# Kernel optimization log

Measured on AMD Instinct MI355X. Metric: run time of the kernel, lower is better.

## Reference

```python
import jax, jax.numpy as jnp
import numpy as np

N = 4096
DIN = 512
H = 128    # hidden_dim per head
K = 4      # num_heads
DOUT = 16  # output classes
ALPHA = 0.2  # leaky relu negative slope


def setup_inputs() -> dict:
    key = jax.random.key(0)
    ks = jax.random.split(key, 8)
    X = jax.random.normal(ks[0], (N, DIN), jnp.float32)
    # sparse random graph (p=0.01), non-zero where edges exist
    adj = (jax.random.uniform(ks[1], (N, N)) < 0.01).astype(jnp.float32)
    W1 = jax.random.normal(ks[2], (K, DIN, H), jnp.float32) * np.float32(1.0 / np.sqrt(DIN))
    a_src1 = jax.random.normal(ks[3], (K, H), jnp.float32) * np.float32(0.1)
    a_dst1 = jax.random.normal(ks[4], (K, H), jnp.float32) * np.float32(0.1)
    W2 = jax.random.normal(ks[5], (K * H, DOUT), jnp.float32) * np.float32(1.0 / np.sqrt(K * H))
    a_src2 = jax.random.normal(ks[6], (DOUT,), jnp.float32) * np.float32(0.1)
    a_dst2 = jax.random.normal(ks[7], (DOUT,), jnp.float32) * np.float32(0.1)
    return {"X": X, "adj": adj, "W1": W1, "a_src1": a_src1, "a_dst1": a_dst1,
            "W2": W2, "a_src2": a_src2, "a_dst2": a_dst2}


def gat_multihead(h, mask, W, a_src, a_dst):
    # h: (N, Din), W: (K, Din, O), a_src/a_dst: (K, O), mask: (N, N) bool
    Wh = jnp.einsum('ni,kio->kno', h, W)                      # (K, N, O)
    src = jnp.einsum('kno,ko->kn', Wh, a_src)                 # (K, N)
    dst = jnp.einsum('kno,ko->kn', Wh, a_dst)                 # (K, N)
    e = jax.nn.leaky_relu(src[:, :, None] + dst[:, None, :], ALPHA)  # (K, N, N)
    e = jnp.where(mask[None], e, -jnp.inf)
    attn = jax.nn.softmax(e, axis=-1)                         # rows sum to 1 (self-loop guarantees >=1 edge)
    return jnp.einsum('knm,kmo->kno', attn, Wh)               # (K, N, O)


def reference(X, adj, W1, a_src1, a_dst1, W2, a_src2, a_dst2):
    # mask = (adj + I) > 0
    mask = (adj + jnp.eye(N, dtype=adj.dtype)) > 0
    # layer 1: 4 heads, concatenated, then ELU (eval mode: no dropout)
    h1 = gat_multihead(X, mask, W1, a_src1, a_dst1)           # (K, N, H)
    h1 = jnp.transpose(h1, (1, 0, 2)).reshape(N, K * H)       # concat heads -> (N, K*H)
    h1 = jax.nn.elu(h1)
    # layer 2: single head, mean over heads == the head itself
    h2 = gat_multihead(h1, mask, W2[None], a_src2[None], a_dst2[None])[0]  # (N, DOUT)
    return jax.nn.log_softmax(h2, axis=1)
```

## Files before the change

### kernel.cpp

```cpp
#include <hip/hip_runtime.h>
#include <hip/hip_bf16.h>
#include <hip/hip_fp16.h>


typedef __attribute__((ext_vector_type(4))) float floatx4;
typedef __attribute__((ext_vector_type(8))) short short8;
typedef __attribute__((ext_vector_type(4))) unsigned short ushortx4;
typedef __attribute__((ext_vector_type(4))) unsigned int uintx4;
typedef unsigned short u16b;

#define GN 4096
#define LDP 40

__device__ __forceinline__ u16b f2bf(float f) {
  union { float f; unsigned int i; } v; v.f = f;
  unsigned int r = v.i + 0x7FFF + ((v.i >> 16) & 1);
  return (u16b)(r >> 16);
}
__device__ __forceinline__ float bflo(unsigned u) {
  union { unsigned i; float f; } v; v.i = u << 16; return v.f;
}
__device__ __forceinline__ float bfhi(unsigned u) {
  union { unsigned i; float f; } v; v.i = u & 0xffff0000u; return v.f;
}
__device__ __forceinline__ float h2f(unsigned short h) {
  return __half2float(__ushort_as_half(h));
}

__global__ __launch_bounds__(512) void k_mask(const float* __restrict__ adj,
                                              u16b* __restrict__ mask) {
  int t = threadIdx.x;
  int n = blockIdx.x * 2 + (t >> 8);
  int cg = t & 255;
  const float* ap = adj + (size_t)n * 4096 + cg * 16;
  floatx4 v0 = *(const floatx4*)(ap);
  floatx4 v1 = *(const floatx4*)(ap + 4);
  floatx4 v2 = *(const floatx4*)(ap + 8);
  floatx4 v3 = *(const floatx4*)(ap + 12);
  unsigned bits = 0;
#pragma unroll
  for (int i = 0; i < 4; ++i) {
    bits |= (unsigned)(v0[i] != 0.f) << i;
    bits |= (unsigned)(v1[i] != 0.f) << (4 + i);
    bits |= (unsigned)(v2[i] != 0.f) << (8 + i);
    bits |= (unsigned)(v3[i] != 0.f) << (12 + i);
  }
  if ((n >> 4) == cg) bits |= 1u << (n & 15);
  mask[(size_t)n * 256 + cg] = (u16b)bits;
}

__global__ __launch_bounds__(512) void k_gemm1(const float* __restrict__ X,
    const float* __restrict__ W1, const float* __restrict__ as1,
    const float* __restrict__ ad1, u16b* __restrict__ Wh1bf,
    float* __restrict__ src1t, float* __restrict__ dst1t) {
  int b = blockIdx.x, t = threadIdx.x;
  int lane = t & 63, w = t >> 6;
  __shared__ u16b Ab[64 * LDP];
  __shared__ u16b Bb[128 * LDP];
  __shared__ float sps[4][64], sds[4][64];
  int p = ((b >> 5) << 3) | (b & 7);
  int hd = (b >> 3) & 3;
  int rb = p * 64;
  const float* Wk = W1 + (size_t)hd * 65536;
  int wr = w >> 2, wc = w & 3, lh = lane >> 4, lm = lane & 15;
  int ar = t >> 2, aq = t & 3;
  int u = t - 256, kk0 = (u & 7) * 4, c0 = (u >> 3) * 4;
  floatx4 pa0, pa1, pb0, pb1, pb2, pb3;
  if (t < 256) {
    const float* ap = X + (size_t)(rb + ar) * 512 + aq * 8;
    pa0 = *(const floatx4*)(ap);
    pa1 = *(const floatx4*)(ap + 4);
  } else {
    const float* bp = Wk + (size_t)kk0 * 128 + c0;
    pb0 = *(const floatx4*)(bp);
    pb1 = *(const floatx4*)(bp + 128);
    pb2 = *(const floatx4*)(bp + 256);
    pb3 = *(const floatx4*)(bp + 384);
  }
  floatx4 acc[2][2] = {};
  for (int kk = 0; kk < 512; kk += 32) {
    if (t < 256) {
      short8 a;
      a[0] = (short)f2bf(pa0[0]); a[1] = (short)f2bf(pa0[1]);
      a[2] = (short)f2bf(pa0[2]); a[3] = (short)f2bf(pa0[3]);
      a[4] = (short)f2bf(pa1[0]); a[5] = (short)f2bf(pa1[1]);
      a[6] = (short)f2bf(pa1[2]); a[7] = (short)f2bf(pa1[3]);
      *(short8*)(&Ab[ar * LDP + aq * 8]) = a;
    } else {
#pragma unroll
      for (int cq = 0; cq < 4; ++cq) {
        ushortx4 v;
        v[0] = f2bf(pb0[cq]); v[1] = f2bf(pb1[cq]);
        v[2] = f2bf(pb2[cq]); v[3] = f2bf(pb3[cq]);
        *(ushortx4*)(&Bb[(c0 + cq) * LDP + kk0]) = v;
      }
    }
    __syncthreads();
    if (kk + 32 < 512) {
      if (t < 256) {
        const float* ap = X + (size_t)(rb + ar) * 512 + kk + 32 + aq * 8;
        pa0 = *(const floatx4*)(ap);
        pa1 = *(const floatx4*)(ap + 4);
      } else {
        const float* bp = Wk + (size_t)(kk + 32 + kk0) * 128 + c0;
        pb0 = *(const floatx4*)(bp);
        pb1 = *(const floatx4*)(bp + 128);
        pb2 = *(const floatx4*)(bp + 256);
        pb3 = *(const floatx4*)(bp + 384);
      }
    }
    short8 a0 = *(const short8*)(&Ab[(wr * 32      + lm) * LDP + lh * 8]);
    short8 a1 = *(const short8*)(&Ab[(wr * 32 + 16 + lm) * LDP + lh * 8]);
    short8 b0 = *(const short8*)(&Bb[(wc * 32      + lm) * LDP + lh * 8]);
    short8 b1 = *(const short8*)(&Bb[(wc * 32 + 16 + lm) * LDP + lh * 8]);
    acc[0][0] = __builtin_amdgcn_mfma_f32_16x16x32_bf16(a0, b0, acc[0][0], 0, 0, 0);
    acc[0][1] = __builtin_amdgcn_mfma_f32_16x16x32_bf16(a0, b1, acc[0][1], 0, 0, 0);
    acc[1][0] = __builtin_amdgcn_mfma_f32_16x16x32_bf16(a1, b0, acc[1][0], 0, 0, 0);
    acc[1][1] = __builtin_amdgcn_mfma_f32_16x16x32_bf16(a1, b1, acc[1][1], 0, 0, 0);
    __syncthreads();
  }
#pragma unroll
  for (int m = 0; m < 2; ++m)
#pragma unroll
    for (int n2 = 0; n2 < 2; ++n2)
#pragma unroll
      for (int j = 0; j < 4; ++j)
        Wh1bf[(size_t)(rb + wr * 32 + m * 16 + lh * 4 + j) * 512
              + hd * 128 + wc * 32 + n2 * 16 + lm] = f2bf(acc[m][n2][j]);
  float asv[2], adv[2];
#pragma unroll
  for (int n2 = 0; n2 < 2; ++n2) {
    asv[n2] = as1[hd * 128 + wc * 32 + n2 * 16 + lm];
    adv[n2] = ad1[hd * 128 + wc * 32 + n2 * 16 + lm];
  }
#pragma unroll
  for (int m = 0; m < 2; ++m)
#pragma unroll
    for (int j = 0; j < 4; ++j) {
      float ps = acc[m][0][j] * asv[0] + acc[m][1][j] * asv[1];
      float pd = acc[m][0][j] * adv[0] + acc[m][1][j] * adv[1];
#pragma unroll
      for (int off = 8; off >= 1; off >>= 1) {
        ps += __shfl_xor(ps, off, 16);
        pd += __shfl_xor(pd, off, 16);
      }
      if (lm == 0) {
        sps[wc][wr * 32 + m * 16 + lh * 4 + j] = ps;
        sds[wc][wr * 32 + m * 16 + lh * 4 + j] = pd;
      }
    }
  __syncthreads();
  if (t < 64) {
    src1t[(size_t)(rb + t) * 4 + hd] = sps[0][t] + sps[1][t] + sps[2][t] + sps[3][t];
    dst1t[(size_t)(rb + t) * 4 + hd] = sds[0][t] + sds[1][t] + sds[2][t] + sds[3][t];
  }
}

__global__ __launch_bounds__(256) void k_attn1(const u16b* __restrict__ mask,
    const u16b* __restrict__ Wh1bf,
    const float* __restrict__ src1t, const float* __restrict__ dst1t,
    const float* __restrict__ W2, const float* __restrict__ as2,
    const float* __restrict__ ad2, float* __restrict__ Wh2,
    float* __restrict__ src2, float* __restrict__ dst2) {
  int w = threadIdx.x >> 6, lane = threadIdx.x & 63;
  int n = blockIdx.x * 4 + w;
  __shared__ u16b lst4[4][512];
  __shared__ unsigned short ewh4[4][2048];
  __shared__ float h1t4[4][512];
  u16b* lst = lst4[w];
  unsigned short* ewh = ewh4[w];
  float* h1t = h1t4[w];
  unsigned long long B = *(const unsigned long long*)((const char*)mask + (size_t)n * 512 + lane * 8);
  int pc = __popcll(B);
  int incl = pc;
#pragma unroll
  for (int off = 1; off <= 32; off <<= 1) {
    int v = __shfl_up(incl, off);
    if (lane >= off) incl += v;
  }
  int cnt = __shfl(incl, 63);
  int pos = incl - pc;
  while (B) {
    int c = __builtin_ctzll(B);
    lst[pos++] = (u16b)(lane * 64 + c);
    B &= B - 1;
  }
  floatx4 sn = *(const floatx4*)(src1t + (size_t)n * 4);
  float mx[4], sm[4];
#pragma unroll
  for (int k = 0; k < 4; ++k) { mx[k] = -1e30f; sm[k] = 0.f; }
  for (int li = lane; li < cnt; li += 64) {
    int m = lst[li];
    floatx4 dv = *(const floatx4*)(dst1t + (size_t)m * 4);
    ushortx4 ev;
#pragma unroll
    for (int k = 0; k < 4; ++k) {
      float e = sn[k] + dv[k];
      e = e > 0.f ? e : 0.2f * e;
      ev[k] = __half_as_ushort(__float2half(e));
      if (e > mx[k]) { sm[k] = sm[k] * __expf(mx[k] - e) + 1.f; mx[k] = e; }
      else sm[k] += __expf(e - mx[k]);
    }
    *(ushortx4*)(&ewh[li * 4]) = ev;
  }
#pragma unroll
  for (int k = 0; k < 4; ++k) {
#pragma unroll
    for (int off = 32; off >= 1; off >>= 1) {
      float mo = __shfl_xor(mx[k], off);
      float so = __shfl_xor(sm[k], off);
      float M = fmaxf(mx[k], mo);
      sm[k] = sm[k] * __expf(mx[k] - M) + so * __expf(mo - M);
      mx[k] = M;
    }
    sm[k] = 1.f / sm[k];
  }
  for (int li = lane; li < cnt; li += 64) {
    ushortx4 ev = *(const ushortx4*)(&ewh[li * 4]);
#pragma unroll
    for (int k = 0; k < 4; ++k) {
      float e = h2f(ev[k]);
      ev[k] = __half_as_ushort(__float2half(__expf(e - mx[k]) * sm[k]));
    }
    *(ushortx4*)(&ewh[li * 4]) = ev;
  }
  int hd = lane >> 4;
  const char* gb = (const char*)Wh1bf + lane * 16;
  float a[8] = {0.f, 0.f, 0.f, 0.f, 0.f, 0.f, 0.f, 0.f};
  int mreg[8];
  float wreg[8];
  int nfull = cnt >> 3;
  if (nfull) {
#pragma unroll
    for (int q = 0; q < 8; ++q) {
      mreg[q] = lst[q];
      wreg[q] = h2f(ewh[q * 4 + hd]);
    }
  }
  for (int c = 0; c < nfull; ++c) {
    uintx4 u0 = *(const uintx4*)(gb + (size_t)mreg[0] * 1024);
    uintx4 u1 = *(const uintx4*)(gb + (size_t)mreg[1] * 1024);
    uintx4 u2 = *(const uintx4*)(gb + (size_t)mreg[2] * 1024);
    uintx4 u3 = *(const uintx4*)(gb + (size_t)mreg[3] * 1024);
    uintx4 u4 = *(const uintx4*)(gb + (size_t)mreg[4] * 1024);
    uintx4 u5 = *(const uintx4*)(gb + (size_t)mreg[5] * 1024);
    uintx4 u6 = *(const uintx4*)(gb + (size_t)mreg[6] * 1024);
    uintx4 u7 = *(const uintx4*)(gb + (size_t)mreg[7] * 1024);
    float f0 = wreg[0], f1 = wreg[1], f2 = wreg[2], f3 = wreg[3];
    float f4 = wreg[4], f5 = wreg[5], f6 = wreg[6], f7 = wreg[7];
    if (c + 1 < nfull) {
      int nb = (c + 1) * 8;
#pragma unroll
      for (int q = 0; q < 8; ++q) {
        mreg[q] = lst[nb + q];
        wreg[q] = h2f(ewh[(nb + q) * 4 + hd]);
      }
    }
#pragma unroll
    for (int j = 0; j < 4; ++j) {
      a[2*j]   = fmaf(f0, bflo(u0[j]), a[2*j]); a[2*j+1] = fmaf(f0, bfhi(u0[j]), a[2*j+1]);
    }
#pragma unroll
    for (int j = 0; j < 4; ++j) {
      a[2*j]   = fmaf(f1, bflo(u1[j]), a[2*j]); a[2*j+1] = fmaf(f1, bfhi(u1[j]), a[2*j+1]);
    }
#pragma unroll
    for (int j = 0; j < 4; ++j) {
      a[2*j]   = fmaf(f2, bflo(u2[j]), a[2*j]); a[2*j+1] = fmaf(f2, bfhi(u2[j]), a[2*j+1]);
    }
#pragma unroll
    for (int j = 0; j < 4; ++j) {
      a[2*j]   = fmaf(f3, bflo(u3[j]), a[2*j]); a[2*j+1] = fmaf(f3, bfhi(u3[j]), a[2*j+1]);
    }
#pragma unroll
    for (int j = 0; j < 4; ++j) {
      a[2*j]   = fmaf(f4, bflo(u4[j]), a[2*j]); a[2*j+1] = fmaf(f4, bfhi(u4[j]), a[2*j+1]);
    }
#pragma unroll
    for (int j = 0; j < 4; ++j) {
      a[2*j]   = fmaf(f5, bflo(u5[j]), a[2*j]); a[2*j+1] = fmaf(f5, bfhi(u5[j]), a[2*j+1]);
    }
#pragma unroll
    for (int j = 0; j < 4; ++j) {
      a[2*j]   = fmaf(f6, bflo(u6[j]), a[2*j]); a[2*j+1] = fmaf(f6, bfhi(u6[j]), a[2*j+1]);
    }
#pragma unroll
    for (int j = 0; j < 4; ++j) {
      a[2*j]   = fmaf(f7, bflo(u7[j]), a[2*j]); a[2*j+1] = fmaf(f7, bfhi(u7[j]), a[2*j+1]);
    }
  }
  for (int li = nfull * 8; li < cnt; ++li) {
    int m = lst[li];
    float wv = h2f(ewh[li * 4 + hd]);
    uintx4 u = *(const uintx4*)(gb + (size_t)m * 1024);
#pragma unroll
    for (int j = 0; j < 4; ++j) {
      a[2*j]   = fmaf(wv, bflo(u[j]), a[2*j]);
      a[2*j+1] = fmaf(wv, bfhi(u[j]), a[2*j+1]);
    }
  }
#pragma unroll
  for (int j = 0; j < 8; ++j) {
    float v = a[j];
    h1t[j * 64 + lane] = v > 0.f ? v : __expf(v) - 1.f;
  }
  int o = lane & 15, ig = lane >> 4;
  float p0 = 0.f, p1 = 0.f, p2 = 0.f, p3 = 0.f;
  for (int j = 0; j < 128; j += 4) {
    int i0 = ig + 4 * j;
    int i1 = i0 + 4, i2 = i0 + 8, i3 = i0 + 12;
    p0 = fmaf(h1t[(i0 & 7) * 64 + (i0 >> 3)], W2[i0 * 16 + o], p0);
    p1 = fmaf(h1t[(i1 & 7) * 64 + (i1 >> 3)], W2[i1 * 16 + o], p1);
    p2 = fmaf(h1t[(i2 & 7) * 64 + (i2 >> 3)], W2[i2 * 16 + o], p2);
    p3 = fmaf(h1t[(i3 & 7) * 64 + (i3 >> 3)], W2[i3 * 16 + o], p3);
  }
  float pacc = (p0 + p1) + (p2 + p3);
  pacc += __shfl_xor(pacc, 16);
  pacc += __shfl_xor(pacc, 32);
  if (lane < 16) {
    Wh2[(size_t)n * 16 + lane] = pacc;
    float ps = pacc * as2[lane];
    float pd = pacc * ad2[lane];
#pragma unroll
    for (int off = 8; off >= 1; off >>= 1) {
      ps += __shfl_xor(ps, off, 16);
      pd += __shfl_xor(pd, off, 16);
    }
    if (lane == 0) { src2[n] = ps; dst2[n] = pd; }
  }
}

__global__ __launch_bounds__(256) void k_attn2(const u16b* __restrict__ mask,
    const float* __restrict__ Wh2, const float* __restrict__ src2,
    const float* __restrict__ dst2, float* __restrict__ out) {
  int w = threadIdx.x >> 6, lane = threadIdx.x & 63;
  int n = blockIdx.x * 4 + w;
  __shared__ int2 pr4[4][512];
  int2* pr = pr4[w];
  float snv = src2[n];
  unsigned long long B = *(const unsigned long long*)((const char*)mask + (size_t)n * 512 + lane * 8);
  int pc = __popcll(B);
  int incl = pc;
#pragma unroll
  for (int off = 1; off <= 32; off <<= 1) {
    int v = __shfl_up(incl, off);
    if (lane >= off) incl += v;
  }
  int cnt = __shfl(incl, 63);
  int pos = incl - pc;
  float mx = -1e30f, sm = 0.f;
  while (B) {
    int c = __builtin_ctzll(B);
    int m = lane * 64 + c;
    float e = snv + dst2[m];
    e = e > 0.f ? e : 0.2f * e;
    if (e > mx) { sm = sm * __expf(mx - e) + 1.f; mx = e; }
    else sm += __expf(e - mx);
    int2 pv; pv.x = m << 4; pv.y = __float_as_int(e);
    pr[pos++] = pv;
    B &= B - 1;
  }
#pragma unroll
  for (int off = 32; off >= 1; off >>= 1) {
    float mo = __shfl_xor(mx, off);
    float so = __shfl_xor(sm, off);
    float M = fmaxf(mx, mo);
    sm = sm * __expf(mx - M) + so * __expf(mo - M);
    mx = M;
  }
  float R = 1.f / sm;
  int o = lane & 15, g = lane >> 4;
  float acc = 0.f;
  for (int li = g; li < cnt; li += 4) {
    int2 pv = pr[li];
    float wgt = __expf(__int_as_float(pv.y) - mx) * R;
    acc = fmaf(wgt, Wh2[pv.x + o], acc);
  }
  acc += __shfl_xor(acc, 16);
  acc += __shfl_xor(acc, 32);
  float vm = acc;
#pragma unroll
  for (int off = 8; off >= 1; off >>= 1) vm = fmaxf(vm, __shfl_xor(vm, off, 16));
  float ex = __expf(acc - vm);
#pragma unroll
  for (int off = 8; off >= 1; off >>= 1) ex += __shfl_xor(ex, off, 16);
  if (lane < 16) out[(size_t)n * 16 + lane] = acc - vm - __logf(ex);
}

extern "C" void kernel_launch(void* const* d_in, const int* in_sizes, int n_in,
                              void* d_out, int out_size, void* d_ws, size_t ws_size,
                              hipStream_t stream) {
  const float* X   = (const float*)d_in[0];
  const float* adj = (const float*)d_in[1];
  const float* W1  = (const float*)d_in[2];
  const float* as1 = (const float*)d_in[3];
  const float* ad1 = (const float*)d_in[4];
  const float* W2  = (const float*)d_in[5];
  const float* as2 = (const float*)d_in[6];
  const float* ad2 = (const float*)d_in[7];
  float* out = (float*)d_out;

  char* ws = (char*)d_ws;
  float* src1t = (float*)ws;
  float* dst1t = (float*)(ws + (64 << 10));
  float* src2  = (float*)(ws + (128 << 10));
  float* dst2  = (float*)(ws + (144 << 10));
  float* Wh2   = (float*)(ws + (160 << 10));
  u16b*  mask  = (u16b*)(ws + (512 << 10));
  u16b*  Wh1bf = (u16b*)(ws + (4ull << 20));

  k_mask <<<dim3(2048), dim3(512), 0, stream>>>(adj, mask);
  k_gemm1<<<dim3(256),  dim3(512), 0, stream>>>(X, W1, as1, ad1, Wh1bf, src1t, dst1t);
  k_attn1<<<dim3(1024), dim3(256), 0, stream>>>(mask, Wh1bf, src1t, dst1t,
                                                W2, as2, ad2, Wh2, src2, dst2);
  k_attn2<<<dim3(1024), dim3(256), 0, stream>>>(mask, Wh2, src2, dst2, out);
}
```

Baseline: 61.63 us.

## Merge mask and GEMM kernels into one launch; double-buffer attn1 gathers

Folds the adjacency-to-bitmask kernel and the layer-1 GEMM into a single launch, with block ranges split by role, so the two independent stages overlap and one launch is saved. In the layer-1 aggregation, the neighbor list is zero-padded to an even number of 8-element chunks, removing the scalar tail loop. The gather loop now keeps two register sets of eight rows, loading the next chunk while the current one is accumulated. This hides gather latency but raises register pressure and does some padded work on row 0 with zero weight.

```diff
diff --git a/kernel.cpp b/kernel.cpp
--- a/kernel.cpp
+++ b/kernel.cpp
@@ -27,132 +27,131 @@
   return __half2float(__ushort_as_half(h));
 }
 
-__global__ __launch_bounds__(512) void k_mask(const float* __restrict__ adj,
-                                              u16b* __restrict__ mask) {
-  int t = threadIdx.x;
-  int n = blockIdx.x * 2 + (t >> 8);
-  int cg = t & 255;
-  const float* ap = adj + (size_t)n * 4096 + cg * 16;
-  floatx4 v0 = *(const floatx4*)(ap);
-  floatx4 v1 = *(const floatx4*)(ap + 4);
-  floatx4 v2 = *(const floatx4*)(ap + 8);
-  floatx4 v3 = *(const floatx4*)(ap + 12);
-  unsigned bits = 0;
-#pragma unroll
-  for (int i = 0; i < 4; ++i) {
-    bits |= (unsigned)(v0[i] != 0.f) << i;
-    bits |= (unsigned)(v1[i] != 0.f) << (4 + i);
-    bits |= (unsigned)(v2[i] != 0.f) << (8 + i);
-    bits |= (unsigned)(v3[i] != 0.f) << (12 + i);
-  }
-  if ((n >> 4) == cg) bits |= 1u << (n & 15);
-  mask[(size_t)n * 256 + cg] = (u16b)bits;
-}
-
-__global__ __launch_bounds__(512) void k_gemm1(const float* __restrict__ X,
-    const float* __restrict__ W1, const float* __restrict__ as1,
-    const float* __restrict__ ad1, u16b* __restrict__ Wh1bf,
+__global__ __launch_bounds__(512) void k_fused1(const float* __restrict__ adj,
+    const float* __restrict__ X, const float* __restrict__ W1,
+    const float* __restrict__ as1, const float* __restrict__ ad1,
+    u16b* __restrict__ mask, u16b* __restrict__ Wh1bf,
     float* __restrict__ src1t, float* __restrict__ dst1t) {
   int b = blockIdx.x, t = threadIdx.x;
   int lane = t & 63, w = t >> 6;
-  __shared__ u16b Ab[64 * LDP];
-  __shared__ u16b Bb[128 * LDP];
-  __shared__ float sps[4][64], sds[4][64];
-  int p = ((b >> 5) << 3) | (b & 7);
-  int hd = (b >> 3) & 3;
-  int rb = p * 64;
-  const float* Wk = W1 + (size_t)hd * 65536;
-  int wr = w >> 2, wc = w & 3, lh = lane >> 4, lm = lane & 15;
-  int ar = t >> 2, aq = t & 3;
-  int u = t - 256, kk0 = (u & 7) * 4, c0 = (u >> 3) * 4;
-  floatx4 pa0, pa1, pb0, pb1, pb2, pb3;
-  if (t < 256) {
-    const float* ap = X + (size_t)(rb + ar) * 512 + aq * 8;
-    pa0 = *(const floatx4*)(ap);
-    pa1 = *(const floatx4*)(ap + 4);
+  if (b >= 256) {
+    int n = (b - 256) * 2 + (t >> 8);
+    int cg = t & 255;
+    const float* ap = adj + (size_t)n * 4096 + cg * 16;
+    floatx4 v0 = *(const floatx4*)(ap);
+    floatx4 v1 = *(const floatx4*)(ap + 4);
+    floatx4 v2 = *(const floatx4*)(ap + 8);
+    floatx4 v3 = *(const floatx4*)(ap + 12);
+    unsigned bits = 0;
+#pragma unroll
+    for (int i = 0; i < 4; ++i) {
+      bits |= (unsigned)(v0[i] != 0.f) << i;
+      bits |= (unsigned)(v1[i] != 0.f) << (4 + i);
+      bits |= (unsigned)(v2[i] != 0.f) << (8 + i);
+      bits |= (unsigned)(v3[i] != 0.f) << (12 + i);
+    }
+    if ((n >> 4) == cg) bits |= 1u << (n & 15);
+    mask[(size_t)n * 256 + cg] = (u16b)bits;
   } else {
-    const float* bp = Wk + (size_t)kk0 * 128 + c0;
-    pb0 = *(const floatx4*)(bp);
-    pb1 = *(const floatx4*)(bp + 128);
-    pb2 = *(const floatx4*)(bp + 256);
-    pb3 = *(const floatx4*)(bp + 384);
-  }
-  floatx4 acc[2][2] = {};
-  for (int kk = 0; kk < 512; kk += 32) {
+    __shared__ u16b Ab[64 * LDP];
+    __shared__ u16b Bb[128 * LDP];
+    __shared__ float sps[4][64], sds[4][64];
+    int p = ((b >> 5) << 3) | (b & 7);
+    int hd = (b >> 3) & 3;
+    int rb = p * 64;
+    const float* Wk = W1 + (size_t)hd * 65536;
+    int wr = w >> 2, wc = w & 3, lh = lane >> 4, lm = lane & 15;
+    int ar = t >> 2, aq = t & 3;
+    int u = t - 256, kk0 = (u & 7) * 4, c0 = (u >> 3) * 4;
+    floatx4 pa0, pa1, pb0, pb1, pb2, pb3;
     if (t < 256) {
-      short8 a;
-      a[0] = (short)f2bf(pa0[0]); a[1] = (short)f2bf(pa0[1]);
-      a[2] = (short)f2bf(pa0[2]); a[3] = (short)f2bf(pa0[3]);
-      a[4] = (short)f2bf(pa1[0]); a[5] = (short)f2bf(pa1[1]);
-      a[6] = (short)f2bf(pa1[2]); a[7] = (short)f2bf(pa1[3]);
-      *(short8*)(&Ab[ar * LDP + aq * 8]) = a;
+      const float* ap = X + (size_t)(rb + ar) * 512 + aq * 8;
+      pa0 = *(const floatx4*)(ap);
+      pa1 = *(const floatx4*)(ap + 4);
     } else {
-#pragma unroll
-      for (int cq = 0; cq < 4; ++cq) {
-        ushortx4 v;
-        v[0] = f2bf(pb0[cq]); v[1] = f2bf(pb1[cq]);
-        v[2] = f2bf(pb2[cq]); v[3] = f2bf(pb3[cq]);
-        *(ushortx4*)(&Bb[(c0 + cq) * LDP + kk0]) = v;
-      }
-    }
+      const float* bp = Wk + (size_t)kk0 * 128 + c0;
+      pb0 = *(const floatx4*)(bp);
+      pb1 = *(const floatx4*)(bp + 128);
+      pb2 = *(const floatx4*)(bp + 256);
+      pb3 = *(const floatx4*)(bp + 384);
+    }
+    floatx4 acc[2][2] = {};
+    for (int kk = 0; kk < 512; kk += 32) {
+      if (t < 256) {
+        short8 a;
+        a[0] = (short)f2bf(pa0[0]); a[1] = (short)f2bf(pa0[1]);
+        a[2] = (short)f2bf(pa0[2]); a[3] = (short)f2bf(pa0[3]);
+        a[4] = (short)f2bf(pa1[0]); a[5] = (short)f2bf(pa1[1]);
+        a[6] = (short)f2bf(pa1[2]); a[7] = (short)f2bf(pa1[3]);
+        *(short8*)(&Ab[ar * LDP + aq * 8]) = a;
+      } else {
+#pragma unroll
+        for (int cq = 0; cq < 4; ++cq) {
+          ushortx4 v;
+          v[0] = f2bf(pb0[cq]); v[1] = f2bf(pb1[cq]);
+          v[2] = f2bf(pb2[cq]); v[3] = f2bf(pb3[cq]);
+          *(ushortx4*)(&Bb[(c0 + cq) * LDP + kk0]) = v;
+        }
+      }
+      __syncthreads();
+      if (kk + 32 < 512) {
+        if (t < 256) {
+          const float* ap = X + (size_t)(rb + ar) * 512 + kk + 32 + aq * 8;
+          pa0 = *(const floatx4*)(ap);
+          pa1 = *(const floatx4*)(ap + 4);
+        } else {
+          const float* bp = Wk + (size_t)(kk + 32 + kk0) * 128 + c0;
+          pb0 = *(const floatx4*)(bp);
+          pb1 = *(const floatx4*)(bp + 128);
+          pb2 = *(const floatx4*)(bp + 256);
+          pb3 = *(const floatx4*)(bp + 384);
+        }
+      }
+      short8 a0 = *(const short8*)(&Ab[(wr * 32      + lm) * LDP + lh * 8]);
+      short8 a1 = *(const short8*)(&Ab[(wr * 32 + 16 + lm) * LDP + lh * 8]);
+      short8 b0 = *(const short8*)(&Bb[(wc * 32      + lm) * LDP + lh * 8]);
+      short8 b1 = *(const short8*)(&Bb[(wc * 32 + 16 + lm) * LDP + lh * 8]);
+      acc[0][0] = __builtin_amdgcn_mfma_f32_16x16x32_bf16(a0, b0, acc[0][0], 0, 0, 0);
+      acc[0][1] = __builtin_amdgcn_mfma_f32_16x16x32_bf16(a0, b1, acc[0][1], 0, 0, 0);
+      acc[1][0] = __builtin_amdgcn_mfma_f32_16x16x32_bf16(a1, b0, acc[1][0], 0, 0, 0);
+      acc[1][1] = __builtin_amdgcn_mfma_f32_16x16x32_bf16(a1, b1, acc[1][1], 0, 0, 0);
+      __syncthreads();
+    }
+#pragma unroll
+    for (int m = 0; m < 2; ++m)
+#pragma unroll
+      for (int n2 = 0; n2 < 2; ++n2)
+#pragma unroll
+        for (int j = 0; j < 4; ++j)
+          Wh1bf[(size_t)(rb + wr * 32 + m * 16 + lh * 4 + j) * 512
+                + hd * 128 + wc * 32 + n2 * 16 + lm] = f2bf(acc[m][n2][j]);
+    float asv[2], adv[2];
+#pragma unroll
+    for (int n2 = 0; n2 < 2; ++n2) {
+      asv[n2] = as1[hd * 128 + wc * 32 + n2 * 16 + lm];
+      adv[n2] = ad1[hd * 128 + wc * 32 + n2 * 16 + lm];
+    }
+#pragma unroll
+    for (int m = 0; m < 2; ++m)
+#pragma unroll
+      for (int j = 0; j < 4; ++j) {
+        float ps = acc[m][0][j] * asv[0] + acc[m][1][j] * asv[1];
+        float pd = acc[m][0][j] * adv[0] + acc[m][1][j] * adv[1];
+#pragma unroll
+        for (int off = 8; off >= 1; off >>= 1) {
+          ps += __shfl_xor(ps, off, 16);
+          pd += __shfl_xor(pd, off, 16);
+        }
+        if (lm == 0) {
+          sps[wc][wr * 32 + m * 16 + lh * 4 + j] = ps;
+          sds[wc][wr * 32 + m * 16 + lh * 4 + j] = pd;
+        }
+      }
     __syncthreads();
-    if (kk + 32 < 512) {
-      if (t < 256) {
-        const float* ap = X + (size_t)(rb + ar) * 512 + kk + 32 + aq * 8;
-        pa0 = *(const floatx4*)(ap);
-        pa1 = *(const floatx4*)(ap + 4);
-      } else {
-        const float* bp = Wk + (size_t)(kk + 32 + kk0) * 128 + c0;
-        pb0 = *(const floatx4*)(bp);
-        pb1 = *(const floatx4*)(bp + 128);
-        pb2 = *(const floatx4*)(bp + 256);
-        pb3 = *(const floatx4*)(bp + 384);
-      }
-    }
-    short8 a0 = *(const short8*)(&Ab[(wr * 32      + lm) * LDP + lh * 8]);
-    short8 a1 = *(const short8*)(&Ab[(wr * 32 + 16 + lm) * LDP + lh * 8]);
-    short8 b0 = *(const short8*)(&Bb[(wc * 32      + lm) * LDP + lh * 8]);
-    short8 b1 = *(const short8*)(&Bb[(wc * 32 + 16 + lm) * LDP + lh * 8]);
-    acc[0][0] = __builtin_amdgcn_mfma_f32_16x16x32_bf16(a0, b0, acc[0][0], 0, 0, 0);
-    acc[0][1] = __builtin_amdgcn_mfma_f32_16x16x32_bf16(a0, b1, acc[0][1], 0, 0, 0);
-    acc[1][0] = __builtin_amdgcn_mfma_f32_16x16x32_bf16(a1, b0, acc[1][0], 0, 0, 0);
-    acc[1][1] = __builtin_amdgcn_mfma_f32_16x16x32_bf16(a1, b1, acc[1][1], 0, 0, 0);
-    __syncthreads();
-  }
-#pragma unroll
-  for (int m = 0; m < 2; ++m)
-#pragma unroll
-    for (int n2 = 0; n2 < 2; ++n2)
-#pragma unroll
-      for (int j = 0; j < 4; ++j)
-        Wh1bf[(size_t)(rb + wr * 32 + m * 16 + lh * 4 + j) * 512
-              + hd * 128 + wc * 32 + n2 * 16 + lm] = f2bf(acc[m][n2][j]);
-  float asv[2], adv[2];
-#pragma unroll
-  for (int n2 = 0; n2 < 2; ++n2) {
-    asv[n2] = as1[hd * 128 + wc * 32 + n2 * 16 + lm];
-    adv[n2] = ad1[hd * 128 + wc * 32 + n2 * 16 + lm];
-  }
-#pragma unroll
-  for (int m = 0; m < 2; ++m)
-#pragma unroll
-    for (int j = 0; j < 4; ++j) {
-      float ps = acc[m][0][j] * asv[0] + acc[m][1][j] * asv[1];
-      float pd = acc[m][0][j] * adv[0] + acc[m][1][j] * adv[1];
-#pragma unroll
-      for (int off = 8; off >= 1; off >>= 1) {
-        ps += __shfl_xor(ps, off, 16);
-        pd += __shfl_xor(pd, off, 16);
-      }
-      if (lm == 0) {
-        sps[wc][wr * 32 + m * 16 + lh * 4 + j] = ps;
-        sds[wc][wr * 32 + m * 16 + lh * 4 + j] = pd;
-      }
-    }
-  __syncthreads();
-  if (t < 64) {
-    src1t[(size_t)(rb + t) * 4 + hd] = sps[0][t] + sps[1][t] + sps[2][t] + sps[3][t];
-    dst1t[(size_t)(rb + t) * 4 + hd] = sds[0][t] + sds[1][t] + sds[2][t] + sds[3][t];
+    if (t < 64) {
+      src1t[(size_t)(rb + t) * 4 + hd] = sps[0][t] + sps[1][t] + sps[2][t] + sps[3][t];
+      dst1t[(size_t)(rb + t) * 4 + hd] = sds[0][t] + sds[1][t] + sds[2][t] + sds[3][t];
+    }
   }
 }
 
@@ -185,6 +184,12 @@
     lst[pos++] = (u16b)(lane * 64 + c);
     B &= B - 1;
   }
+  int nch = (cnt + 7) >> 3;
+  int nch2 = nch + (nch & 1);
+  for (int i = cnt + lane; i < nch2 * 8; i += 64) {
+    lst[i] = 0;
+    *(unsigned long long*)(&ewh[i * 4]) = 0ull;
+  }
   floatx4 sn = *(const floatx4*)(src1t + (size_t)n * 4);
   float mx[4], sm[4];
 #pragma unroll
@@ -227,76 +232,46 @@
   int hd = lane >> 4;
   const char* gb = (const char*)Wh1bf + lane * 16;
   float a[8] = {0.f, 0.f, 0.f, 0.f, 0.f, 0.f, 0.f, 0.f};
-  int mreg[8];
-  float wreg[8];
-  int nfull = cnt >> 3;
-  if (nfull) {
+  int ma[8]; float wa[8]; uintx4 A[8];
+#pragma unroll
+  for (int q = 0; q < 8; ++q) { ma[q] = lst[q]; wa[q] = h2f(ewh[q * 4 + hd]); }
+#pragma unroll
+  for (int q = 0; q < 8; ++q) A[q] = *(const uintx4*)(gb + (size_t)ma[q] * 1024);
+  for (int c = 0; c < nch2; c += 2) {
+    int mb[8]; float wb[8]; uintx4 Bv[8];
 #pragma unroll
     for (int q = 0; q < 8; ++q) {
-      mreg[q] = lst[q];
-      wreg[q] = h2f(ewh[q * 4 + hd]);
-    }
-  }
-  for (int c = 0; c < nfull; ++c) {
-    uintx4 u0 = *(const uintx4*)(gb + (size_t)mreg[0] * 1024);
-    uintx4 u1 = *(const uintx4*)(gb + (size_t)mreg[1] * 1024);
-    uintx4 u2 = *(const uintx4*)(gb + (size_t)mreg[2] * 1024);
-    uintx4 u3 = *(const uintx4*)(gb + (size_t)mreg[3] * 1024);
-    uintx4 u4 = *(const uintx4*)(gb + (size_t)mreg[4] * 1024);
-    uintx4 u5 = *(const uintx4*)(gb + (size_t)mreg[5] * 1024);
-    uintx4 u6 = *(const uintx4*)(gb + (size_t)mreg[6] * 1024);
-    uintx4 u7 = *(const uintx4*)(gb + (size_t)mreg[7] * 1024);
-    float f0 = wreg[0], f1 = wreg[1], f2 = wreg[2], f3 = wreg[3];
-    float f4 = wreg[4], f5 = wreg[5], f6 = wreg[6], f7 = wreg[7];
-    if (c + 1 < nfull) {
-      int nb = (c + 1) * 8;
+      int li = (c + 1) * 8 + q;
+      mb[q] = lst[li]; wb[q] = h2f(ewh[li * 4 + hd]);
+    }
+#pragma unroll
+    for (int q = 0; q < 8; ++q) Bv[q] = *(const uintx4*)(gb + (size_t)mb[q] * 1024);
+#pragma unroll
+    for (int q = 0; q < 8; ++q) {
+      float f = wa[q];
+#pragma unroll
+      for (int j = 0; j < 4; ++j) {
+        a[2*j]   = fmaf(f, bflo(A[q][j]), a[2*j]);
+        a[2*j+1] = fmaf(f, bfhi(A[q][j]), a[2*j+1]);
+      }
+    }
+    if (c + 2 < nch2) {
 #pragma unroll
       for (int q = 0; q < 8; ++q) {
-        mreg[q] = lst[nb + q];
-        wreg[q] = h2f(ewh[(nb + q) * 4 + hd]);
-      }
-    }
-#pragma unroll
-    for (int j = 0; j < 4; ++j) {
-      a[2*j]   = fmaf(f0, bflo(u0[j]), a[2*j]); a[2*j+1] = fmaf(f0, bfhi(u0[j]), a[2*j+1]);
-    }
-#pragma unroll
-    for (int j = 0; j < 4; ++j) {
-      a[2*j]   = fmaf(f1, bflo(u1[j]), a[2*j]); a[2*j+1] = fmaf(f1, bfhi(u1[j]), a[2*j+1]);
-    }
-#pragma unroll
-    for (int j = 0; j < 4; ++j) {
-      a[2*j]   = fmaf(f2, bflo(u2[j]), a[2*j]); a[2*j+1] = fmaf(f2, bfhi(u2[j]), a[2*j+1]);
-    }
-#pragma unroll
-    for (int j = 0; j < 4; ++j) {
-      a[2*j]   = fmaf(f3, bflo(u3[j]), a[2*j]); a[2*j+1] = fmaf(f3, bfhi(u3[j]), a[2*j+1]);
-    }
-#pragma unroll
-    for (int j = 0; j < 4; ++j) {
-      a[2*j]   = fmaf(f4, bflo(u4[j]), a[2*j]); a[2*j+1] = fmaf(f4, bfhi(u4[j]), a[2*j+1]);
-    }
-#pragma unroll
-    for (int j = 0; j < 4; ++j) {
-      a[2*j]   = fmaf(f5, bflo(u5[j]), a[2*j]); a[2*j+1] = fmaf(f5, bfhi(u5[j]), a[2*j+1]);
-    }
-#pragma unroll
-    for (int j = 0; j < 4; ++j) {
-      a[2*j]   = fmaf(f6, bflo(u6[j]), a[2*j]); a[2*j+1] = fmaf(f6, bfhi(u6[j]), a[2*j+1]);
-    }
-#pragma unroll
-    for (int j = 0; j < 4; ++j) {
-      a[2*j]   = fmaf(f7, bflo(u7[j]), a[2*j]); a[2*j+1] = fmaf(f7, bfhi(u7[j]), a[2*j+1]);
-    }
-  }
-  for (int li = nfull * 8; li < cnt; ++li) {
-    int m = lst[li];
-    float wv = h2f(ewh[li * 4 + hd]);
-    uintx4 u = *(const uintx4*)(gb + (size_t)m * 1024);
-#pragma unroll
-    for (int j = 0; j < 4; ++j) {
-      a[2*j]   = fmaf(wv, bflo(u[j]), a[2*j]);
-      a[2*j+1] = fmaf(wv, bfhi(u[j]), a[2*j+1]);
+        int li = (c + 2) * 8 + q;
+        ma[q] = lst[li]; wa[q] = h2f(ewh[li * 4 + hd]);
+      }
+#pragma unroll
+      for (int q = 0; q < 8; ++q) A[q] = *(const uintx4*)(gb + (size_t)ma[q] * 1024);
+    }
+#pragma unroll
+    for (int q = 0; q < 8; ++q) {
+      float f = wb[q];
+#pragma unroll
+      for (int j = 0; j < 4; ++j) {
+        a[2*j]   = fmaf(f, bflo(Bv[q][j]), a[2*j]);
+        a[2*j+1] = fmaf(f, bfhi(Bv[q][j]), a[2*j+1]);
+      }
     }
   }
 #pragma unroll
@@ -409,8 +384,8 @@
   u16b*  mask  = (u16b*)(ws + (512 << 10));
   u16b*  Wh1bf = (u16b*)(ws + (4ull << 20));
 
-  k_mask <<<dim3(2048), dim3(512), 0, stream>>>(adj, mask);
-  k_gemm1<<<dim3(256),  dim3(512), 0, stream>>>(X, W1, as1, ad1, Wh1bf, src1t, dst1t);
+  k_fused1<<<dim3(2304), dim3(512), 0, stream>>>(adj, X, W1, as1, ad1,
+                                                 mask, Wh1bf, src1t, dst1t);
   k_attn1<<<dim3(1024), dim3(256), 0, stream>>>(mask, Wh1bf, src1t, dst1t,
                                                 W2, as2, ad2, Wh2, src2, dst2);
   k_attn2<<<dim3(1024), dim3(256), 0, stream>>>(mask, Wh2, src2, dst2, out);
```

New measurement: 57.57 us. 1.07x faster.
